# Kernel optimization log

Hardware: AMD Instinct MI355X
Metric: run time of the kernel (lower is better)

## Reference

```python
import jax, jax.numpy as jnp
import numpy as np

EPS = 1e-6  # LayerNorm epsilon


def setup_inputs() -> dict:
    key = jax.random.key(0)
    ks = jax.random.split(key, 12)
    B, S, T, E = 8, 2048, 2048, 512
    sc = 1.0 / np.sqrt(E)
    inp = {
        "encoder_outputs": jax.random.normal(ks[0], (B, S, E), jnp.float32),
        "emotion": jax.random.normal(ks[1], (B, T, E), jnp.float32),
        "mask": jax.random.randint(ks[2], (B, S, T), 0, 2).astype(bool),
        "Wq": jax.random.normal(ks[3], (E, E), jnp.float32) * sc,
        "bq": jnp.zeros((E,), jnp.float32),
        "Wk": jax.random.normal(ks[4], (E, E), jnp.float32) * sc,
        "bk": jnp.zeros((E,), jnp.float32),
        "Wv": jax.random.normal(ks[5], (E, E), jnp.float32) * sc,
        "bv": jnp.zeros((E,), jnp.float32),
        "Wo": jax.random.normal(ks[6], (E, E), jnp.float32) * sc,
        "gamma": jnp.ones((E,), jnp.float32),
        "beta": jnp.zeros((E,), jnp.float32),
    }
    return inp


def reference(encoder_outputs, emotion, mask, Wq, bq, Wk, bk, Wv, bv, Wo, gamma, beta):
    # Linear projections (torch Linear: x @ W.T + b)
    q = encoder_outputs @ Wq.T + bq          # [B,S,E]
    k = emotion @ Wk.T + bk                  # [B,T,E]
    v = emotion @ Wv.T + bv                  # [B,T,E]
    logits = jnp.einsum("bse,bte->bst", q, k)  # [B,S,T]
    logits = jnp.where(mask, jnp.float32(-1e18), logits)
    weights = jax.nn.softmax(logits, axis=-1)   # dropout1 = identity (eval)
    contexts = jnp.einsum("bst,bte->bse", weights, v)
    attn = contexts @ Wo.T                   # output_linear, no bias
    attn = encoder_outputs + attn            # dropout2 = identity (eval)
    # LayerNorm (std-based, as in common hand-rolled LayerNorm)
    mean = attn.mean(-1, keepdims=True)
    std = attn.std(-1, keepdims=True)
    context = gamma * (attn - mean) / (std + EPS) + beta
    context = encoder_outputs + context      # dropout3 = identity (eval)
    return context
```

## Files before the change

kernel.cpp:

```cpp
#include <hip/hip_runtime.h>
#include <math.h>
#include <stdint.h>


#define BB 8
#define SS 2048
#define TT 2048
#define EE 512

typedef __attribute__((ext_vector_type(8))) short short8;
typedef __attribute__((ext_vector_type(4))) float f32x4;

__device__ __forceinline__ uint16_t f2bf(float f) {
  uint32_t u = __builtin_bit_cast(uint32_t, f);
  u += 0x7fffu + ((u >> 16) & 1u);
  return (uint16_t)(u >> 16);
}
__device__ __forceinline__ float bf2f(uint16_t h) {
  uint32_t u = ((uint32_t)h) << 16;
  return __builtin_bit_cast(float, u);
}

__device__ __forceinline__ size_t toff(int row, int col, int ld) {
  return (size_t)(row >> 4) * ((size_t)ld << 4) + ((size_t)(col >> 3) << 7)
       + ((row & 15) << 3) + (col & 7);
}

__device__ __forceinline__ void gld16(const void* g, void* l) {
  __builtin_amdgcn_global_load_lds(
      (const __attribute__((address_space(1))) void*)g,
      (__attribute__((address_space(3))) void*)l, 16, 0, 0);
}

template<int ASRC, int BSRC, int EPI, int WN>
__global__ __launch_bounds__(256, 2) void mgemm(
    const void* __restrict__ Ap, const void* __restrict__ Alo,
    const void* __restrict__ Bp, const void* __restrict__ Blo,
    void* __restrict__ Cp, void* __restrict__ C2,
    const float* __restrict__ bias, const float* __restrict__ bias2,
    const float* __restrict__ resid,
    const int* __restrict__ mask, float* __restrict__ sZ,
    int K, int lda, int ldb, int ldc,
    size_t sA, size_t sB, size_t sC, size_t sM)
{
  constexpr bool ALOARR = (ASRC == 0);
  constexpr bool BLOARR = (BSRC == 0);
  constexpr bool T3     = (ASRC == 0) && (BSRC == 0);
  constexpr bool T2     = (ASRC == 0) && (BSRC == 1);
  constexpr int  BN     = 32 * WN;
  constexpr int  ABYTES = ALOARR ? 16384 : 8192;
  constexpr int  BBYTES = BLOARR ? BN * 128 : BN * 64;

  __shared__ char smem[ABYTES + BBYTES];

  const int tid  = threadIdx.x;
  const int lane = tid & 63, wv = tid >> 6;
  const int z    = blockIdx.z;
  const int bm   = blockIdx.y * 128;
  const int bn   = blockIdx.x * BN;
  const int fr   = lane & 15;
  const int wm   = (wv & 1) * 64;
  const int wn   = (wv >> 1) * (16 * WN);

  const f32x4 zero = {0.f, 0.f, 0.f, 0.f};
  f32x4 acc[4][WN];
#pragma unroll
  for (int i = 0; i < 4; ++i)
#pragma unroll
    for (int j = 0; j < WN; ++j) acc[i][j] = zero;

  const size_t loff = (size_t)lane * 8;
  const uint16_t* gAh = (const uint16_t*)Ap + sA * z + (size_t)(bm >> 4) * 16 * lda + loff;
  const uint16_t* gAl = ALOARR ? (const uint16_t*)Alo + sA * z + (size_t)(bm >> 4) * 16 * lda + loff : nullptr;
  const uint16_t* gBh = (const uint16_t*)Bp + sB * z + (size_t)(bn >> 4) * 16 * ldb + loff;
  const uint16_t* gBl = BLOARR ? (const uint16_t*)Blo + sB * z + (size_t)(bn >> 4) * 16 * ldb + loff : nullptr;

  for (int k0 = 0; k0 < K; k0 += 32) {
    const size_t ka = (size_t)k0 * 16;
    __syncthreads();
#pragma unroll
    for (int t = 0; t < 2; ++t) { int s = wv + t * 4;
      gld16(gAh + (size_t)s * 16 * lda + ka, &smem[s * 1024]); }
    if constexpr (ALOARR) {
#pragma unroll
      for (int t = 0; t < 2; ++t) { int s = wv + t * 4;
        gld16(gAl + (size_t)s * 16 * lda + ka, &smem[8192 + s * 1024]); }
    }
#pragma unroll
    for (int t = 0; t < WN / 2; ++t) { int s = wv + t * 4;
      gld16(gBh + (size_t)s * 16 * ldb + ka, &smem[ABYTES + s * 1024]); }
    if constexpr (BLOARR) {
#pragma unroll
      for (int t = 0; t < WN / 2; ++t) { int s = wv + t * 4;
        gld16(gBl + (size_t)s * 16 * ldb + ka, &smem[ABYTES + BN * 64 + s * 1024]); }
    }
    __syncthreads();

    short8 ah[4], bh[WN], al_[4], bl_[WN];
#pragma unroll
    for (int i = 0; i < 4; ++i) {
      const char* p = smem + ((wm >> 4) + i) * 1024 + (lane << 4);
      ah[i] = *(const short8*)p;
      if constexpr (ALOARR) al_[i] = *(const short8*)(p + 8192);
    }
#pragma unroll
    for (int j = 0; j < WN; ++j) {
      const char* p = smem + ABYTES + ((wn >> 4) + j) * 1024 + (lane << 4);
      bh[j] = *(const short8*)p;
      if constexpr (BLOARR) bl_[j] = *(const short8*)(p + BN * 64);
    }
#pragma unroll
    for (int i = 0; i < 4; ++i)
#pragma unroll
      for (int j = 0; j < WN; ++j) {
        acc[i][j] = __builtin_amdgcn_mfma_f32_16x16x32_bf16(ah[i], bh[j], acc[i][j], 0, 0, 0);
        if constexpr (T3) {
          acc[i][j] = __builtin_amdgcn_mfma_f32_16x16x32_bf16(ah[i], bl_[j], acc[i][j], 0, 0, 0);
          acc[i][j] = __builtin_amdgcn_mfma_f32_16x16x32_bf16(al_[i], bh[j], acc[i][j], 0, 0, 0);
        } else if constexpr (T2) {
          acc[i][j] = __builtin_amdgcn_mfma_f32_16x16x32_bf16(al_[i], bh[j], acc[i][j], 0, 0, 0);
        }
      }
  }

  if constexpr (EPI == 5) {
#pragma unroll
    for (int i = 0; i < 4; ++i) {
      const int row0 = bm + wm + i * 16 + (lane >> 4) * 4;
#pragma unroll
      for (int g = 0; g < 4; ++g) {
        const int row = row0 + g;
        float rs = 0.f;
#pragma unroll
        for (int j = 0; j < WN; ++j) {
          const int col = bn + wn + j * 16 + fr;
          const bool msk = mask[sM * z + (size_t)row * ldc + col] != 0;
          const float e = msk ? 0.f : __expf(acc[i][j][g] - 60.0f);
          ((uint16_t*)Cp)[sC * z + toff(row, col, ldc)] = f2bf(e);
          rs += e;
        }
        rs += __shfl_xor(rs, 1);
        rs += __shfl_xor(rs, 2);
        rs += __shfl_xor(rs, 4);
        rs += __shfl_xor(rs, 8);
        if ((lane & 15) == 0) atomicAdd(&sZ[(size_t)z * SS + row], rs);
      }
    }
  } else {
#pragma unroll
    for (int i = 0; i < 4; ++i) {
      const int row0 = bm + wm + i * 16 + (lane >> 4) * 4;
#pragma unroll
      for (int g = 0; g < 4; ++g) {
        const int row = row0 + g;
        float invZ = 1.0f;
        if constexpr (EPI == 6) invZ = 1.0f / sZ[(size_t)z * SS + row];
#pragma unroll
        for (int j = 0; j < WN; ++j) {
          const int col = bn + wn + j * 16 + fr;
          float v = acc[i][j][g];
          if constexpr (EPI == 0) {
            const float* bp = (z == 0) ? bias : bias2;
            const size_t ci = sC * z + toff(row, col, ldc);
            v += bp[col];
            uint16_t h = f2bf(v);
            ((uint16_t*)Cp)[ci] = h;
            ((uint16_t*)C2)[ci] = f2bf(v - bf2f(h));
          } else if constexpr (EPI == 1) {
            v += bias[row];
            ((uint16_t*)Cp)[sC * z + toff(row, col, ldc)] = f2bf(v);
          } else if constexpr (EPI == 4) {
            v += resid[(size_t)row * ldc + col];
            ((float*)Cp)[sC * z + (size_t)row * ldc + col] = v;
          } else {
            ((uint16_t*)Cp)[sC * z + toff(row, col, ldc)] = f2bf(v * invZ);
          }
        }
      }
    }
  }
}

__device__ __forceinline__ void split_core(
    const float* __restrict__ x, uint16_t* __restrict__ hi,
    uint16_t* __restrict__ lo, int bid)
{
  __shared__ uint16_t lh[256 * 8 + 16 * 8];
  __shared__ uint16_t ll[256 * 8 + 16 * 8];
  const int t   = threadIdx.x;
  const int seg = bid >> 2, q = bid & 3;

  const float* src = x + (size_t)(seg * 16 + (t >> 4)) * 512 + q * 128 + (t & 15) * 8;
  float4 a = *(const float4*)src;
  float4 b = *(const float4*)(src + 4);
  float v[8] = {a.x, a.y, a.z, a.w, b.x, b.y, b.z, b.w};

  const int slot = (t & 15) * 16 + (t >> 4);
  uint16_t* ph = lh + slot * 8 + (slot >> 4) * 8;
  uint16_t* pl = ll + slot * 8 + (slot >> 4) * 8;
#pragma unroll
  for (int e = 0; e < 8; ++e) {
    uint16_t h = f2bf(v[e]);
    ph[e] = h;
    pl[e] = f2bf(v[e] - bf2f(h));
  }
  __syncthreads();

  const uint16_t* qh = lh + t * 8 + (t >> 4) * 8;
  const uint16_t* ql = ll + t * 8 + (t >> 4) * 8;
  const size_t off = (size_t)seg * 8192 + (size_t)(q * 16 + (t >> 4)) * 128 + (t & 15) * 8;
  *(short8*)(hi + off) = *(const short8*)qh;
  *(short8*)(lo + off) = *(const short8*)ql;
}

__global__ __launch_bounds__(256) void split_pair(
    const float* __restrict__ x0, const float* __restrict__ x1,
    uint16_t* __restrict__ hi, uint16_t* __restrict__ lo, size_t stride)
{
  const int sel = blockIdx.x >> 12;
  const int bid = blockIdx.x & 4095;
  split_core(sel ? x1 : x0, hi + sel * stride, lo + sel * stride, bid);
}

__global__ __launch_bounds__(256) void split_w4(
    const float* __restrict__ x0, const float* __restrict__ x1,
    const float* __restrict__ x2, const float* __restrict__ x3,
    uint16_t* __restrict__ hi0, uint16_t* __restrict__ lo0, size_t stride)
{
  const int w   = blockIdx.x >> 7;
  const int bid = blockIdx.x & 127;
  const float* x = (w == 0) ? x0 : (w == 1) ? x1 : (w == 2) ? x2 : x3;
  split_core(x, hi0 + w * stride, lo0 + w * stride, bid);
}

__global__ __launch_bounds__(256) void ln_kernel(
    const float* __restrict__ X, const float* __restrict__ enc,
    const float* __restrict__ gamma, const float* __restrict__ beta,
    float* __restrict__ out)
{
  const int row = blockIdx.x * 4 + (threadIdx.x >> 6);
  const int lane = threadIdx.x & 63;
  const size_t base = (size_t)row * EE;
  const int o0 = lane * 4, o1 = 256 + lane * 4;

  float4 x0 = *(const float4*)(X + base + o0);
  float4 x1 = *(const float4*)(X + base + o1);
  float s = x0.x + x0.y + x0.z + x0.w + x1.x + x1.y + x1.z + x1.w;
#pragma unroll
  for (int off = 32; off > 0; off >>= 1) s += __shfl_xor(s, off);
  const float mean = s * (1.0f / 512.0f);

  float d[8] = {x0.x - mean, x0.y - mean, x0.z - mean, x0.w - mean,
                x1.x - mean, x1.y - mean, x1.z - mean, x1.w - mean};
  float s2 = 0.f;
#pragma unroll
  for (int i = 0; i < 8; ++i) s2 = fmaf(d[i], d[i], s2);
#pragma unroll
  for (int off = 32; off > 0; off >>= 1) s2 += __shfl_xor(s2, off);
  const float stdv = sqrtf(s2 * (1.0f / 512.0f));
  const float inv = 1.0f / (stdv + 1e-6f);

  float4 g0 = *(const float4*)(gamma + o0);
  float4 g1 = *(const float4*)(gamma + o1);
  float4 b0 = *(const float4*)(beta + o0);
  float4 b1 = *(const float4*)(beta + o1);
  float4 e0 = *(const float4*)(enc + base + o0);
  float4 e1 = *(const float4*)(enc + base + o1);

  float4 r0, r1;
  r0.x = e0.x + g0.x * d[0] * inv + b0.x;
  r0.y = e0.y + g0.y * d[1] * inv + b0.y;
  r0.z = e0.z + g0.z * d[2] * inv + b0.z;
  r0.w = e0.w + g0.w * d[3] * inv + b0.w;
  r1.x = e1.x + g1.x * d[4] * inv + b1.x;
  r1.y = e1.y + g1.y * d[5] * inv + b1.y;
  r1.z = e1.z + g1.z * d[6] * inv + b1.z;
  r1.w = e1.w + g1.w * d[7] * inv + b1.w;
  *(float4*)(out + base + o0) = r0;
  *(float4*)(out + base + o1) = r1;
}

extern "C" void kernel_launch(void* const* d_in, const int* in_sizes, int n_in,
                              void* d_out, int out_size, void* d_ws, size_t ws_size,
                              hipStream_t stream) {
  const float* enc   = (const float*)d_in[0];
  const float* emo   = (const float*)d_in[1];
  const int*   mask  = (const int*)d_in[2];
  const float* Wq    = (const float*)d_in[3];
  const float* bq    = (const float*)d_in[4];
  const float* Wk    = (const float*)d_in[5];
  const float* bk    = (const float*)d_in[6];
  const float* Wv    = (const float*)d_in[7];
  const float* bv    = (const float*)d_in[8];
  const float* Wo    = (const float*)d_in[9];
  const float* gamma = (const float*)d_in[10];
  const float* beta  = (const float*)d_in[11];
  float* out = (float*)d_out;
  char*  ws  = (char*)d_ws;

  const size_t SZ = (size_t)BB * SS * EE;
  size_t off = 0;
  uint16_t* enc_h = (uint16_t*)(ws + off); off += SZ * 2;
  uint16_t* enc_l = (uint16_t*)(ws + off); off += SZ * 2;
  uint16_t* emo_h = (uint16_t*)(ws + off); off += SZ * 2;
  uint16_t* emo_l = (uint16_t*)(ws + off); off += SZ * 2;
  uint16_t* q_hi  = (uint16_t*)(ws + off); off += SZ * 2;
  uint16_t* q_lo  = (uint16_t*)(ws + off); off += SZ * 2;
  uint16_t* k_hi  = (uint16_t*)(ws + off); off += SZ * 2;
  uint16_t* k_lo  = (uint16_t*)(ws + off); off += SZ * 2;
  uint16_t* vT    = (uint16_t*)(ws + off); off += SZ * 2;
  uint16_t* ctx   = (uint16_t*)(ws + off); off += SZ * 2;
  uint16_t* wq_h  = (uint16_t*)(ws + off); off += EE * EE * 2;
  uint16_t* wq_l  = (uint16_t*)(ws + off); off += EE * EE * 2;
  uint16_t* wk_h  = (uint16_t*)(ws + off); off += EE * EE * 2;
  uint16_t* wk_l  = (uint16_t*)(ws + off); off += EE * EE * 2;
  uint16_t* wv_h  = (uint16_t*)(ws + off); off += EE * EE * 2;
  uint16_t* wv_l  = (uint16_t*)(ws + off); off += EE * EE * 2;
  uint16_t* wo_h  = (uint16_t*)(ws + off); off += EE * EE * 2;
  uint16_t* wo_l  = (uint16_t*)(ws + off); off += EE * EE * 2;
  uint16_t* P_u   = (uint16_t*)(ws + off); off += (size_t)BB * SS * TT * 2;
  float*    sZ    = (float*)(ws + off);    off += (size_t)BB * SS * 4;
  (void)k_lo; (void)wk_l; (void)wv_l; (void)wo_l;

  const dim3 blk(256);

  split_w4<<<dim3(512), blk, 0, stream>>>(Wq, Wk, Wv, Wo, wq_h, wq_l,
                                          (size_t)2 * EE * EE);
  split_pair<<<dim3(8192), blk, 0, stream>>>(enc, emo, enc_h, enc_l,
                                             (size_t)2 * SZ);
  hipMemsetAsync(sZ, 0, (size_t)BB * SS * 4, stream);

  mgemm<0, 0, 0, 4><<<dim3(4, 128, 2), blk, 0, stream>>>(
      enc_h, enc_l, wq_h, wq_l, q_hi, q_lo, bq, bk, nullptr, nullptr, nullptr,
      EE, EE, EE, EE, 2 * SZ, (size_t)2 * EE * EE, 2 * SZ, 0);
  mgemm<1, 1, 1, 4><<<dim3(128, 4, 1), blk, 0, stream>>>(
      wv_h, nullptr, emo_h, nullptr, vT, nullptr, bv, nullptr, nullptr,
      nullptr, nullptr, EE, EE, EE, BB * TT, 0, 0, 0, 0);

  mgemm<0, 1, 5, 4><<<dim3(16, 16, 8), blk, 0, stream>>>(
      q_hi, q_lo, k_hi, nullptr, P_u, nullptr, nullptr, nullptr, nullptr,
      mask, sZ, EE, EE, EE, TT,
      (size_t)SS * EE, (size_t)TT * EE, (size_t)SS * TT, (size_t)SS * TT);

  mgemm<1, 1, 6, 4><<<dim3(4, 16, 8), blk, 0, stream>>>(
      P_u, nullptr, vT, nullptr, ctx, nullptr, nullptr, nullptr, nullptr,
      nullptr, sZ, TT, TT, BB * TT, EE,
      (size_t)SS * TT, (size_t)TT * 16, (size_t)SS * EE, 0);

  mgemm<1, 1, 4, 4><<<dim3(4, 128, 1), blk, 0, stream>>>(
      ctx, nullptr, wo_h, nullptr, out, nullptr, nullptr, nullptr, enc,
      nullptr, nullptr, EE, EE, EE, EE, 0, 0, 0, 0);
  ln_kernel<<<dim3(BB * SS / 4), blk, 0, stream>>>(out, enc, gamma, beta, out);
}
```

Before: 532.8 us.

## Pack attention mask into bitwords in split kernel and read bits in QK epilogue

Adds blocks to the split kernel that pack the int mask into 64-bit ballot words, stored in the unused k_lo buffer. The QK^T softmax epilogue then loads one 64-bit word per row instead of a scattered int per element. The goal is cheaper, better-coalesced mask reads in the epilogue, paid for by an extra full read of the mask during the packing pass. It also skips writing the low half of K in the projection epilogue, since that buffer is now reused for the mask bits.

```diff
diff --git a/kernel.cpp b/kernel.cpp
--- a/kernel.cpp
+++ b/kernel.cpp
@@ -124,6 +124,17 @@
   }
 
   if constexpr (EPI == 5) {
+    const unsigned long long* __restrict__ mb = (const unsigned long long*)mask;
+    const size_t mrow = (size_t)TT >> 6;
+    const size_t mbase = (size_t)z * SS * mrow + ((size_t)(bn + wn) >> 6);
+    unsigned long long mw[4][4];
+#pragma unroll
+    for (int i = 0; i < 4; ++i)
+#pragma unroll
+      for (int g = 0; g < 4; ++g) {
+        const int row = bm + wm + i * 16 + (lane >> 4) * 4 + g;
+        mw[i][g] = mb[mbase + (size_t)row * mrow];
+      }
 #pragma unroll
     for (int i = 0; i < 4; ++i) {
       const int row0 = bm + wm + i * 16 + (lane >> 4) * 4;
@@ -134,7 +145,7 @@
 #pragma unroll
         for (int j = 0; j < WN; ++j) {
           const int col = bn + wn + j * 16 + fr;
-          const bool msk = mask[sM * z + (size_t)row * ldc + col] != 0;
+          const bool msk = (mw[i][g] >> (j * 16 + fr)) & 1ull;
           const float e = msk ? 0.f : __expf(acc[i][j][g] - 60.0f);
           ((uint16_t*)Cp)[sC * z + toff(row, col, ldc)] = f2bf(e);
           rs += e;
@@ -165,7 +176,7 @@
             v += bp[col];
             uint16_t h = f2bf(v);
             ((uint16_t*)Cp)[ci] = h;
-            ((uint16_t*)C2)[ci] = f2bf(v - bf2f(h));
+            if (z == 0) ((uint16_t*)C2)[ci] = f2bf(v - bf2f(h));
           } else if constexpr (EPI == 1) {
             v += bias[row];
             ((uint16_t*)Cp)[sC * z + toff(row, col, ldc)] = f2bf(v);
@@ -215,8 +226,20 @@
 
 __global__ __launch_bounds__(256) void split_pair(
     const float* __restrict__ x0, const float* __restrict__ x1,
-    uint16_t* __restrict__ hi, uint16_t* __restrict__ lo, size_t stride)
-{
+    uint16_t* __restrict__ hi, uint16_t* __restrict__ lo, size_t stride,
+    const int* __restrict__ mask, unsigned long long* __restrict__ mbits)
+{
+  if (blockIdx.x >= 8192) {
+    const int lane = threadIdx.x & 63;
+    const size_t wid = ((size_t)(blockIdx.x - 8192) * 256 + threadIdx.x) >> 6;
+    const size_t nwords = (size_t)BB * SS * TT / 64;
+    for (size_t w = wid; w < nwords; w += 2048 * 4) {
+      const int m = mask[(w << 6) + lane];
+      const unsigned long long b = __ballot(m != 0);
+      if (lane == 0) mbits[w] = b;
+    }
+    return;
+  }
   const int sel = blockIdx.x >> 12;
   const int bid = blockIdx.x & 4095;
   split_core(sel ? x1 : x0, hi + sel * stride, lo + sel * stride, bid);
@@ -320,14 +343,16 @@
   uint16_t* wo_l  = (uint16_t*)(ws + off); off += EE * EE * 2;
   uint16_t* P_u   = (uint16_t*)(ws + off); off += (size_t)BB * SS * TT * 2;
   float*    sZ    = (float*)(ws + off);    off += (size_t)BB * SS * 4;
-  (void)k_lo; (void)wk_l; (void)wv_l; (void)wo_l;
+  (void)wk_l; (void)wv_l; (void)wo_l;
+
+  unsigned long long* mbits = (unsigned long long*)k_lo;
 
   const dim3 blk(256);
 
   split_w4<<<dim3(512), blk, 0, stream>>>(Wq, Wk, Wv, Wo, wq_h, wq_l,
                                           (size_t)2 * EE * EE);
-  split_pair<<<dim3(8192), blk, 0, stream>>>(enc, emo, enc_h, enc_l,
-                                             (size_t)2 * SZ);
+  split_pair<<<dim3(8192 + 2048), blk, 0, stream>>>(enc, emo, enc_h, enc_l,
+                                                    (size_t)2 * SZ, mask, mbits);
   hipMemsetAsync(sZ, 0, (size_t)BB * SS * 4, stream);
 
   mgemm<0, 0, 0, 4><<<dim3(4, 128, 2), blk, 0, stream>>>(
@@ -339,8 +364,8 @@
 
   mgemm<0, 1, 5, 4><<<dim3(16, 16, 8), blk, 0, stream>>>(
       q_hi, q_lo, k_hi, nullptr, P_u, nullptr, nullptr, nullptr, nullptr,
-      mask, sZ, EE, EE, EE, TT,
-      (size_t)SS * EE, (size_t)TT * EE, (size_t)SS * TT, (size_t)SS * TT);
+      (const int*)mbits, sZ, EE, EE, EE, TT,
+      (size_t)SS * EE, (size_t)TT * EE, (size_t)SS * TT, 0);
 
   mgemm<1, 1, 6, 4><<<dim3(4, 16, 8), blk, 0, stream>>>(
       P_u, nullptr, vT, nullptr, ctx, nullptr, nullptr, nullptr, nullptr,
```

Measured after the change: 542.2 us. Within noise of the previous version (+1.8%).

## Prefetch mask tile into LDS bitmask during K loop of logits GEMM

Applied to the files above, without the earlier changes.

In the exp/logit epilogue kernel, the int mask tile is read with coalesced int4 loads spread across K-loop iterations, compressed via ballots into 64-bit words in shared memory, and then decoded per element in the epilogue. This replaces scattered per-element global mask reads at the end of the kernel with bit tests on LDS. The projection epilogue also skips writing the low-half bf16 split for the second batch slice (z != 0). The approach relies on the K loop having enough iterations to cover all 128 rows and on a specific tile width, so it is tied to the tile shape.

```diff
diff --git a/kernel.cpp b/kernel.cpp
--- a/kernel.cpp
+++ b/kernel.cpp
@@ -52,6 +52,7 @@
   constexpr int  BBYTES = BLOARR ? BN * 128 : BN * 64;
 
   __shared__ char smem[ABYTES + BBYTES];
+  __shared__ unsigned long long pm[(EPI == 5) ? 256 : 1];
 
   const int tid  = threadIdx.x;
   const int lane = tid & 63, wv = tid >> 6;
@@ -77,6 +78,7 @@
 
   for (int k0 = 0; k0 < K; k0 += 32) {
     const size_t ka = (size_t)k0 * 16;
+    const int r = k0 >> 5;
     __syncthreads();
 #pragma unroll
     for (int t = 0; t < 2; ++t) { int s = wv + t * 4;
@@ -94,7 +96,23 @@
       for (int t = 0; t < WN / 2; ++t) { int s = wv + t * 4;
         gld16(gBl + (size_t)s * 16 * ldb + ka, &smem[ABYTES + BN * 64 + s * 1024]); }
     }
+    int4 mm;
+    if constexpr (EPI == 5)
+      mm = *(const int4*)(mask + sM * z + (size_t)(bm + r * 8 + (tid >> 5)) * ldc
+                               + bn + (tid & 31) * 4);
     __syncthreads();
+
+    if constexpr (EPI == 5) {
+      const unsigned long long b0 = __ballot(mm.x != 0);
+      const unsigned long long b1 = __ballot(mm.y != 0);
+      const unsigned long long b2 = __ballot(mm.z != 0);
+      const unsigned long long b3 = __ballot(mm.w != 0);
+      if (lane < 4) {
+        const unsigned long long w64 = (lane == 0) ? b0 : (lane == 1) ? b1
+                                     : (lane == 2) ? b2 : b3;
+        pm[(r * 4 + wv) * 4 + lane] = w64;
+      }
+    }
 
     short8 ah[4], bh[WN], al_[4], bl_[WN];
 #pragma unroll
@@ -124,17 +142,28 @@
   }
 
   if constexpr (EPI == 5) {
+    __syncthreads();
+    const int sh0 = (wn >> 6) * 16 + (fr >> 2);
+    unsigned long long mw[4][4];
+#pragma unroll
+    for (int i = 0; i < 4; ++i)
+#pragma unroll
+      for (int g = 0; g < 4; ++g) {
+        const int lrow = wm + i * 16 + (lane >> 4) * 4 + g;
+        mw[i][g] = pm[(lrow >> 1) * 4 + (fr & 3)];
+      }
 #pragma unroll
     for (int i = 0; i < 4; ++i) {
       const int row0 = bm + wm + i * 16 + (lane >> 4) * 4;
 #pragma unroll
       for (int g = 0; g < 4; ++g) {
         const int row = row0 + g;
+        const int sh  = sh0 + (g & 1) * 32;
         float rs = 0.f;
 #pragma unroll
         for (int j = 0; j < WN; ++j) {
           const int col = bn + wn + j * 16 + fr;
-          const bool msk = mask[sM * z + (size_t)row * ldc + col] != 0;
+          const bool msk = (mw[i][g] >> (sh + j * 4)) & 1ull;
           const float e = msk ? 0.f : __expf(acc[i][j][g] - 60.0f);
           ((uint16_t*)Cp)[sC * z + toff(row, col, ldc)] = f2bf(e);
           rs += e;
@@ -165,7 +194,7 @@
             v += bp[col];
             uint16_t h = f2bf(v);
             ((uint16_t*)Cp)[ci] = h;
-            ((uint16_t*)C2)[ci] = f2bf(v - bf2f(h));
+            if (z == 0) ((uint16_t*)C2)[ci] = f2bf(v - bf2f(h));
           } else if constexpr (EPI == 1) {
             v += bias[row];
             ((uint16_t*)Cp)[sC * z + toff(row, col, ldc)] = f2bf(v);
```

New measurement: 535.0 us. Within noise of the previous version (+0.4%).
